# Optimization experiments

Hardware: AMD Instinct MI355X
Metric: run time of the kernel (lower is better)

Reference implementation:

```python
import jax, jax.numpy as jnp
import numpy as np

B, T, D, K, DEPTH = 8, 1024, 128, 64, 1


def _rel_ids(T, k):
    # relative_mat_id[i, j] = clamp(k + j - i, 0, 2k)
    base = jnp.arange(k, k + T)[None, :] - jnp.arange(T)[:, None]
    return jnp.clip(base, 0, 2 * k)  # [T, T] int32


def setup_inputs() -> dict:
    key = jax.random.key(0)
    ks = jax.random.split(key, 13)
    s = 1.0 / np.sqrt(D)
    return {
        "x": jax.random.normal(ks[0], (B, T, D), dtype=jnp.float32),
        "W0": jax.random.normal(ks[1], (D, D), dtype=jnp.float32) * s,
        "b0": jnp.zeros((D,), dtype=jnp.float32),
        "Wq": jax.random.normal(ks[2], (D, D), dtype=jnp.float32) * s,
        "bq": jnp.zeros((D,), dtype=jnp.float32),
        "Wk": jax.random.normal(ks[3], (D, D), dtype=jnp.float32) * s,
        "bk": jnp.zeros((D,), dtype=jnp.float32),
        "Wv": jax.random.normal(ks[4], (D, D), dtype=jnp.float32) * s,
        "bv": jnp.zeros((D,), dtype=jnp.float32),
        "W1": jax.random.normal(ks[5], (D, D), dtype=jnp.float32) * s,
        "b1": jnp.zeros((D,), dtype=jnp.float32),
        "pe_key": jax.random.normal(ks[6], (2 * K + 1, D), dtype=jnp.float32) * np.sqrt(2.0 / (2 * K + 1)),
        "pe_value": jax.random.normal(ks[7], (2 * K + 1, D), dtype=jnp.float32) * np.sqrt(2.0 / (2 * K + 1)),
    }


def reference(x, W0, b0, Wq, bq, Wk, bk, Wv, bv, W1, b1, pe_key, pe_value):
    Tlen = x.shape[1]
    ids = _rel_ids(Tlen, K)                     # [T, T]
    rpr_key = pe_key[ids]                       # [T, T, D]
    rpr_value = pe_value[ids]                   # [T, T, D]

    hs = jax.nn.relu(x @ W0 + b0)               # fc0 (dropout = eval identity)
    for _ in range(DEPTH):
        q = jnp.tanh(hs @ Wq + bq)
        k = jnp.tanh(hs @ Wk + bk)
        v = jnp.tanh(hs @ Wv + bv)
        a = jnp.einsum("bid,bjd->bij", q, k)
        a = a + jnp.einsum("ijd,bid->bij", rpr_key, q)
        a = jax.nn.softmax(a, axis=2)
        c = jnp.einsum("bij,bjd->bid", a, v)
        c = c + jnp.einsum("bij,ijd->bid", a, rpr_value)
        hs = jax.nn.relu(c @ W1 + b1)
    return hs
```

## Files before the change

kernel.cpp:

```cpp
#include <hip/hip_runtime.h>


#define TT 1024
#define DD 128
#define NB 8
#define SJH 1160

typedef _Float16 f16;
typedef __attribute__((ext_vector_type(8))) _Float16 f16x8;
typedef __attribute__((ext_vector_type(4))) _Float16 f16x4;
typedef __attribute__((ext_vector_type(4))) float f32x4;

static __device__ inline float fast_tanh(float x) {
    float xc = fminf(fmaxf(x, -12.f), 12.f);
    float e = __expf(2.f * xc);
    return (e - 1.f) / (e + 1.f);
}

#define GLDS(gp, lp) __builtin_amdgcn_global_load_lds( \
    (const __attribute__((address_space(1))) unsigned*)(gp), \
    (__attribute__((address_space(3))) unsigned*)(lp), 16, 0, 0)

__global__ __launch_bounds__(256) void prep_w(
        const float* __restrict__ W0, const float* __restrict__ Wq,
        const float* __restrict__ Wk, const float* __restrict__ Wv,
        const float* __restrict__ W1, char* __restrict__ wimg) {
    const int blk = blockIdx.x, t = threadIdx.x;
    const float* W = blk == 0 ? W0 : blk == 1 ? Wq : blk == 2 ? Wk
                   : blk == 3 ? Wv : W1;
    char* o = wimg + (size_t)blk * 32768;
    #pragma unroll
    for (int it = 0; it < 8; it++) {
        int item = t + 256 * it;
        int n = item & 127, k0 = (item >> 7) * 8;
        f16x8 h;
        #pragma unroll
        for (int e = 0; e < 8; e++) h[e] = (f16)W[(k0 + e) * 128 + n];
        *(f16x8*)(o + n * 256 + ((2 * k0) ^ ((n & 7) << 4))) = h;
    }
}

#define ZACC() do { _Pragma("unroll") for (int _i = 0; _i < 2; _i++) \
    _Pragma("unroll") for (int _j = 0; _j < 2; _j++) \
        acc[_i][_j] = (f32x4){0.f, 0.f, 0.f, 0.f}; } while (0)

#define GEMMCORE(SRC, WL) do { \
    _Pragma("unroll") for (int _c = 0; _c < 4; _c++) { \
        f16x8 _af[2], _bf[2]; \
        _Pragma("unroll") for (int _it = 0; _it < 2; _it++) { \
            int _row = _it * 16 + (l & 15); \
            int _a = (_row << 8) + (_c << 6) + ((l >> 4) << 4); \
            _af[_it] = *(const f16x8*)((SRC) + (_a ^ ((_row & 7) << 4))); } \
        _Pragma("unroll") for (int _nt = 0; _nt < 2; _nt++) { \
            int _n = wv * 32 + _nt * 16 + (l & 15); \
            int _a = (_n << 8) + (_c << 6) + ((l >> 4) << 4); \
            _bf[_nt] = *(const f16x8*)((WL) + (_a ^ ((_n & 7) << 4))); } \
        _Pragma("unroll") for (int _it = 0; _it < 2; _it++) \
        _Pragma("unroll") for (int _nt = 0; _nt < 2; _nt++) \
            acc[_it][_nt] = __builtin_amdgcn_mfma_f32_16x16x32_f16( \
                    _af[_it], _bf[_nt], acc[_it][_nt], 0, 0, 0); } } while (0)

#define ISSUEW(wi, dst) do { \
    const char* _g = wimg + (size_t)(wi) * 32768 + t * 16; \
    char* _d = (dst) + t * 16; \
    _Pragma("unroll") for (int _i = 0; _i < 8; _i++) \
        GLDS(_g + _i * 4096, _d + _i * 4096); \
} while (0)

#define WAITBAR(N) do { \
    asm volatile("s_waitcnt vmcnt(" #N ") lgkmcnt(0)" ::: "memory"); \
    __builtin_amdgcn_s_barrier(); \
    __builtin_amdgcn_sched_barrier(0); \
} while (0)

__global__ __launch_bounds__(256) void fused_qkv(
        const float* __restrict__ x, const char* __restrict__ wimg,
        const float* __restrict__ b0, const float* __restrict__ bq,
        const float* __restrict__ bk, const float* __restrict__ bv,
        const float* __restrict__ PEK, const float* __restrict__ PEV,
        f16* __restrict__ q16, char* __restrict__ kimg,
        char* __restrict__ vimg, char* __restrict__ pekimg,
        char* __restrict__ pevimg) {
    extern __shared__ __align__(16) char smq[];
    char* xs  = smq;
    char* hsl = smq + 8192;
    char* wA  = smq + 16384;
    char* wB  = smq + 49152;
    char* wC  = smq + 81920;
    const int t = threadIdx.x, wv = t >> 6, l = t & 63;
    const int blk = blockIdx.x;

    if (blk >= 256) {
        if (blk == 256) {
            for (int it = 0; it < 64; it++) {
                int idx = t + 256 * it;
                int m = idx >> 7, d = idx & 127;
                *(f16*)(pekimg + (m >> 6) * 16384 + (m & 63) * 256
                        + ((2 * d) ^ ((m & 7) << 4))) = (f16)PEK[m * 128 + d];
            }
        } else {
            for (int it = 0; it < 64; it++) {
                int idx = t + 256 * it;
                int m = idx >> 7, d = idx & 127;
                *(f16*)(pevimg + (m >> 6) * 16384 + d * 128
                        + ((2 * (m & 63)) ^ ((d & 7) << 4))) = (f16)PEV[m * 128 + d];
            }
        }
        return;
    }

    const int r0 = (blk & 7) * 1024 + (blk >> 3) * 32;
    ISSUEW(0, wA);
    ISSUEW(1, wB);
    {
        const float* X = x + (size_t)r0 * 128;
        #pragma unroll
        for (int i = 0; i < 2; i++) {
            f32x4 a0 = *(const f32x4*)(X + t * 16 + i * 8);
            f32x4 a1 = *(const f32x4*)(X + t * 16 + i * 8 + 4);
            f16x8 h;
            h[0]=(f16)a0[0]; h[1]=(f16)a0[1]; h[2]=(f16)a0[2]; h[3]=(f16)a0[3];
            h[4]=(f16)a1[0]; h[5]=(f16)a1[1]; h[6]=(f16)a1[2]; h[7]=(f16)a1[3];
            int a = t * 32 + i * 16;
            *(f16x8*)(xs + (a ^ (((a >> 8) & 7) << 4))) = h;
        }
    }
    WAITBAR(8);

    f32x4 acc[2][2];
    ZACC();
    GEMMCORE(xs, wA);
    {
        #pragma unroll
        for (int it = 0; it < 2; it++)
            #pragma unroll
            for (int nt = 0; nt < 2; nt++) {
                int n = wv * 32 + nt * 16 + (l & 15);
                float bb = b0[n];
                #pragma unroll
                for (int r = 0; r < 4; r++) {
                    int i = it * 16 + (l >> 4) * 4 + r;
                    float v = fmaxf(acc[it][nt][r] + bb, 0.f);
                    int a = i * 256 + 2 * n;
                    *(f16*)(hsl + (a ^ ((i & 7) << 4))) = (f16)v;
                }
            }
    }
    ISSUEW(2, wC);
    WAITBAR(8);

    ZACC();
    GEMMCORE(hsl, wB);
    {
        #pragma unroll
        for (int it = 0; it < 2; it++)
            #pragma unroll
            for (int nt = 0; nt < 2; nt++) {
                int n = wv * 32 + nt * 16 + (l & 15);
                float bb = bq[n];
                #pragma unroll
                for (int r = 0; r < 4; r++) {
                    int i = it * 16 + (l >> 4) * 4 + r;
                    q16[(size_t)(r0 + i) * 128 + n] =
                            (f16)fast_tanh(acc[it][nt][r] + bb);
                }
            }
    }
    ISSUEW(3, wA);
    WAITBAR(8);

    ZACC();
    GEMMCORE(hsl, wC);
    f16* ts = (f16*)xs;
    {
        #pragma unroll
        for (int it = 0; it < 2; it++)
            #pragma unroll
            for (int nt = 0; nt < 2; nt++) {
                int n = wv * 32 + nt * 16 + (l & 15);
                float bb = bk[n];
                #pragma unroll
                for (int r = 0; r < 4; r++) {
                    int i = it * 16 + (l >> 4) * 4 + r;
                    ts[i * 128 + n] = (f16)fast_tanh(acc[it][nt][r] + bb);
                }
            }
    }
    WAITBAR(0);

    {
        #pragma unroll
        for (int half = 0; half < 2; half++) {
            int row = (t >> 4) + half * 16;
            int seg = t & 15;
            int jg = r0 + row;
            int chunk = ((jg >> 10) << 4) + ((jg & 1023) >> 6);
            int jp = jg & 63;
            char* dst = kimg + (size_t)chunk * 16384 + jp * 256
                      + ((seg * 16) ^ ((jp & 7) << 4));
            *(f16x8*)dst = *(const f16x8*)&ts[row * 128 + seg * 8];
        }
    }
    ZACC();
    GEMMCORE(hsl, wA);
    {
        #pragma unroll
        for (int it = 0; it < 2; it++)
            #pragma unroll
            for (int nt = 0; nt < 2; nt++) {
                int d = wv * 32 + nt * 16 + (l & 15);
                float bb = bv[d];
                f16x4 h;
                #pragma unroll
                for (int r = 0; r < 4; r++)
                    h[r] = (f16)fast_tanh(acc[it][nt][r] + bb);
                int jb = r0 + it * 16 + ((l >> 4) << 2);
                int chunk = ((jb >> 10) << 4) + ((jb & 1023) >> 6);
                char* dst = vimg + (size_t)chunk * 16384 + d * 128
                          + ((2 * (jb & 63)) ^ ((d & 7) << 4));
                *(f16x4*)dst = h;
            }
    }
}

#define ISSUE16(src, bi) do { const char* _g = (src) + t * 16; \
    char* _d = BUF + (size_t)(bi) * 16384 + t * 16; \
    GLDS(_g, _d); \
    GLDS(_g + 8192, _d + 8192); \
} while (0)

__global__ __launch_bounds__(512) void attn_all(
        const f16* __restrict__ q16, const char* __restrict__ kimg,
        const char* __restrict__ pekimg, const char* __restrict__ vimg,
        const char* __restrict__ pevimg, const float* __restrict__ PEK,
        const float* __restrict__ PEV, const char* __restrict__ w1img,
        const float* __restrict__ b1, float* __restrict__ out) {
    extern __shared__ __align__(16) char sm7[];
    f16*   S   = (f16*)sm7;
    char*  BUF = sm7 + 74240;
    f16*   QB  = (f16*)(sm7 + 139776);
    float* LR  = (float*)(sm7 + 148224);

    const int t = threadIdx.x, wv = t >> 6, l = t & 63;
    const int lr = l & 15, lg = l >> 4;
    const int b = blockIdx.x & 7;
    const int i0 = (blockIdx.x >> 3) << 5;
    const int it16 = (wv & 1) << 4;
    const int jsub = wv >> 1;

    f16x8 qf[4];
    {
        const f16* qb = q16 + (size_t)(b * TT + i0 + it16 + lr) * 128 + lg * 8;
        #pragma unroll
        for (int c = 0; c < 4; c++) qf[c] = *(const f16x8*)(qb + c * 32);
    }
    const int row2 = t >> 4, l16 = t & 15;
    f16x8 qpv = *(const f16x8*)(q16 + (size_t)(b * TT + i0 + row2) * 128 + l16 * 8);
    f32x4 pkv0 = *(const f32x4*)(PEK + 128 * 128 + l16 * 8);
    f32x4 pkv1 = *(const f32x4*)(PEK + 128 * 128 + l16 * 8 + 4);
    f32x4 pvr4 = *(const f32x4*)(PEV + 128 * 128 + wv * 16 + lg * 4);
    const float bb1 = b1[wv * 16 + lr];

    const char* kbase = kimg + (size_t)b * 16 * 16384;
    const char* vbase = vimg + (size_t)b * 16 * 16384;

    ISSUE16(kbase, 0);
    ISSUE16(kbase + 16384, 1);
    ISSUE16(kbase + 2 * 16384, 2);

    for (int ch = 0; ch < 18; ch++) {
        asm volatile("s_waitcnt vmcnt(4)" ::: "memory");
        __builtin_amdgcn_s_barrier();
        __builtin_amdgcn_sched_barrier(0);
        {
            int ci = ch + 3;
            const char* src = ci < 16 ? kbase + (size_t)ci * 16384
                            : (ci < 18 ? pekimg + (size_t)(ci - 16) * 16384
                                       : vbase + (size_t)(ci - 18) * 16384);
            ISSUE16(src, ci & 3);
        }
        const char* kb = BUF + (size_t)(ch & 3) * 16384;
        const int jp = jsub * 16 + lr;
        f32x4 acc = {0.f, 0.f, 0.f, 0.f};
        #pragma unroll
        for (int c = 0; c < 4; c++) {
            f16x8 kf = *(const f16x8*)(kb + jp * 256
                        + ((c * 64 + lg * 16) ^ ((jp & 7) << 4)));
            acc = __builtin_amdgcn_mfma_f32_16x16x32_f16(kf, qf[c], acc, 0, 0, 0);
        }
        f16x4 h = {(f16)acc[0], (f16)acc[1], (f16)acc[2], (f16)acc[3]};
        *(f16x4*)&S[(it16 + lr) * SJH + ch * 64 + jsub * 16 + lg * 4] = h;
    }
    asm volatile("s_waitcnt lgkmcnt(0)" ::: "memory");
    __builtin_amdgcn_s_barrier();
    __builtin_amdgcn_sched_barrier(0);

    {
        const int ig = i0 + row2;
        f16* srow = S + row2 * SJH;
        f16* qrow = QB + row2 * 132;

        float qp;
        {
            float s = 0.f;
            #pragma unroll
            for (int e = 0; e < 4; e++) s += (float)qpv[e] * pkv0[e];
            #pragma unroll
            for (int e = 0; e < 4; e++) s += (float)qpv[e + 4] * pkv1[e];
            #pragma unroll
            for (int off = 8; off; off >>= 1) s += __shfl_xor(s, off, 64);
            qp = s;
        }
        for (int mm = l16; mm < 128; mm += 16) {
            qrow[mm] = srow[1024 + mm];
            srow[1024 + mm] = (f16)0.f;
        }
        if (l16 == 0) qrow[128] = (f16)qp;
        const float qlo = (float)qrow[0], qhi = qp;

        float lmax = -3.0e38f;
        #pragma unroll
        for (int kk = 0; kk < 8; kk++) {
            int j0 = kk * 128 + l16 * 8;
            f16x8 sv = *(const f16x8*)(srow + j0);
            #pragma unroll
            for (int e = 0; e < 8; e++) {
                int idd = 64 + j0 + e - ig;
                float qv = (idd <= 0) ? qlo : (idd >= 128 ? qhi : (float)qrow[idd]);
                lmax = fmaxf(lmax, (float)sv[e] + qv);
            }
        }
        #pragma unroll
        for (int off = 8; off; off >>= 1) lmax = fmaxf(lmax, __shfl_xor(lmax, off, 64));

        float lsum = 0.f, s0 = 0.f, s1 = 0.f;
        #pragma unroll
        for (int kk = 0; kk < 8; kk++) {
            int j0 = kk * 128 + l16 * 8;
            f16x8 sv = *(const f16x8*)(srow + j0);
            f16x8 pv;
            #pragma unroll
            for (int e = 0; e < 8; e++) {
                int idd = 64 + j0 + e - ig;
                float qv = (idd <= 0) ? qlo : (idd >= 128 ? qhi : (float)qrow[idd]);
                float p = __expf((float)sv[e] + qv - lmax);
                pv[e] = (f16)p;
                lsum += p;
                if (idd <= 0)        s0 += p;
                else if (idd >= 128) s1 += p;
                else                 srow[1024 + idd] = (f16)p;
            }
            *(f16x8*)(srow + j0) = pv;
        }
        #pragma unroll
        for (int off = 8; off; off >>= 1) {
            lsum += __shfl_xor(lsum, off, 64);
            s0   += __shfl_xor(s0,   off, 64);
            s1   += __shfl_xor(s1,   off, 64);
        }
        if (l16 == 0) {
            srow[1024] = (f16)s0;
            srow[1152] = (f16)s1;
            LR[row2] = lsum;
        }
    }
    asm volatile("s_waitcnt lgkmcnt(0)" ::: "memory");
    __builtin_amdgcn_s_barrier();
    __builtin_amdgcn_sched_barrier(0);

    f32x4 cacc[2] = {};
    for (int ch = 0; ch < 18; ch++) {
        if (ch <= 15)      asm volatile("s_waitcnt vmcnt(4)" ::: "memory");
        else if (ch == 16) asm volatile("s_waitcnt vmcnt(2)" ::: "memory");
        else               asm volatile("s_waitcnt vmcnt(0)" ::: "memory");
        __builtin_amdgcn_s_barrier();
        __builtin_amdgcn_sched_barrier(0);
        if (ch < 15) {
            int ci = ch + 3;
            const char* src = ci < 16 ? vbase + (size_t)ci * 16384
                                      : pevimg + (size_t)(ci - 16) * 16384;
            ISSUE16(src, (ci + 2) & 3);
        } else if (ch == 17) {
            const char* _g = w1img + t * 16;
            char* _d = BUF + t * 16;
            #pragma unroll
            for (int _i = 0; _i < 4; _i++)
                GLDS(_g + _i * 8192, _d + _i * 8192);
        }
        const char* vb = BUF + (size_t)((ch + 2) & 3) * 16384;
        const int dp = wv * 16 + lr;
        #pragma unroll
        for (int c2 = 0; c2 < 2; c2++) {
            f16x8 vf = *(const f16x8*)(vb + dp * 128
                        + ((c2 * 64 + lg * 16) ^ ((dp & 7) << 4)));
            #pragma unroll
            for (int i2 = 0; i2 < 2; i2++) {
                f16x8 pf = *(const f16x8*)&S[(i2 * 16 + lr) * SJH
                            + ch * 64 + c2 * 32 + lg * 8];
                cacc[i2] = __builtin_amdgcn_mfma_f32_16x16x32_f16(vf, pf, cacc[i2], 0, 0, 0);
            }
        }
    }

    float w128[2], rden[2];
    #pragma unroll
    for (int i2 = 0; i2 < 2; i2++) {
        int irow = i2 * 16 + lr;
        w128[i2] = (float)S[irow * SJH + 1152];
        rden[i2] = 1.f / LR[irow];
    }
    asm volatile("s_waitcnt lgkmcnt(0)" ::: "memory");
    __builtin_amdgcn_s_barrier();
    __builtin_amdgcn_sched_barrier(0);
    char* cl = (char*)S;
    {
        #pragma unroll
        for (int i2 = 0; i2 < 2; i2++) {
            int i = i2 * 16 + lr;
            #pragma unroll
            for (int r = 0; r < 4; r++) {
                int d = wv * 16 + lg * 4 + r;
                float cv = (cacc[i2][r] + w128[i2] * pvr4[r]) * rden[i2];
                int a = i * 256 + 2 * d;
                *(f16*)(cl + (a ^ ((i & 7) << 4))) = (f16)cv;
            }
        }
    }
    asm volatile("s_waitcnt vmcnt(0) lgkmcnt(0)" ::: "memory");
    __builtin_amdgcn_s_barrier();
    __builtin_amdgcn_sched_barrier(0);

    const char* wl4 = BUF;
    f32x4 oacc[2] = {};
    #pragma unroll
    for (int c = 0; c < 4; c++) {
        f16x8 af[2], bf;
        #pragma unroll
        for (int i2 = 0; i2 < 2; i2++) {
            int row = i2 * 16 + lr;
            int a = (row << 8) + (c << 6) + (lg << 4);
            af[i2] = *(const f16x8*)(cl + (a ^ ((row & 7) << 4)));
        }
        {
            int n = wv * 16 + lr;
            int a = (n << 8) + (c << 6) + (lg << 4);
            bf = *(const f16x8*)(wl4 + (a ^ ((n & 7) << 4)));
        }
        #pragma unroll
        for (int i2 = 0; i2 < 2; i2++)
            oacc[i2] = __builtin_amdgcn_mfma_f32_16x16x32_f16(af[i2], bf, oacc[i2], 0, 0, 0);
    }
    {
        int n = wv * 16 + lr;
        #pragma unroll
        for (int i2 = 0; i2 < 2; i2++) {
            #pragma unroll
            for (int r = 0; r < 4; r++) {
                int i = i2 * 16 + lg * 4 + r;
                out[(size_t)(b * TT + i0 + i) * DD + n] = fmaxf(oacc[i2][r] + bb1, 0.f);
            }
        }
    }
}


extern "C" void kernel_launch(void* const* d_in, const int* in_sizes, int n_in,
                              void* d_out, int out_size, void* d_ws, size_t ws_size,
                              hipStream_t stream) {
    const float* x   = (const float*)d_in[0];
    const float* W0  = (const float*)d_in[1];
    const float* b0  = (const float*)d_in[2];
    const float* Wq  = (const float*)d_in[3];
    const float* bq  = (const float*)d_in[4];
    const float* Wk  = (const float*)d_in[5];
    const float* bk  = (const float*)d_in[6];
    const float* Wv  = (const float*)d_in[7];
    const float* bv  = (const float*)d_in[8];
    const float* W1  = (const float*)d_in[9];
    const float* b1  = (const float*)d_in[10];
    const float* pek = (const float*)d_in[11];
    const float* pev = (const float*)d_in[12];
    float* out = (float*)d_out;

    const size_t NTD = (size_t)NB * TT * DD;
    f16* q16 = (f16*)d_ws;
    char* wimg   = (char*)(q16 + NTD);
    char* kimg   = wimg + 5 * 32768;
    char* vimg   = kimg + (size_t)128 * 16384;
    char* pekimg = vimg + (size_t)128 * 16384;
    char* pevimg = pekimg + 32768;

    const int SMEM_QKV  = 114688;
    const int SMEM_ATTN = 148352;
    hipFuncSetAttribute(reinterpret_cast<const void*>(fused_qkv),
                        hipFuncAttributeMaxDynamicSharedMemorySize, SMEM_QKV);
    hipFuncSetAttribute(reinterpret_cast<const void*>(attn_all),
                        hipFuncAttributeMaxDynamicSharedMemorySize, SMEM_ATTN);

    hipLaunchKernelGGL(prep_w, dim3(5), dim3(256), 0, stream,
                       W0, Wq, Wk, Wv, W1, wimg);
    hipLaunchKernelGGL(fused_qkv, dim3(258), dim3(256), SMEM_QKV, stream,
                       x, wimg, b0, bq, bk, bv, pek, pev,
                       q16, kimg, vimg, pekimg, pevimg);
    hipLaunchKernelGGL(attn_all, dim3(256), dim3(512), SMEM_ATTN, stream,
                       q16, kimg, pekimg, vimg, pevimg, pek, pev,
                       wimg + 4 * 32768, b1, out);
}
```

Baseline: 51.82 us.

## Fuse QKV projection and attention into one kernel with a grid barrier

Merges the QKV projection kernel and the attention kernel into a single 512-thread persistent kernel. Q stays in LDS instead of round-tripping through global memory, and a device-wide atomic-counter barrier makes sure all K/V images are written before the attention phase starts. The PE image conversion moves into the weight-prep kernel. This removes a kernel launch and the Q global traffic, but it depends on all 256 blocks being co-resident, which could deadlock otherwise, and it adds a memset launch plus spin-wait cost.

```diff
diff --git a/kernel.cpp b/kernel.cpp
--- a/kernel.cpp
+++ b/kernel.cpp
@@ -21,207 +21,68 @@
     (const __attribute__((address_space(1))) unsigned*)(gp), \
     (__attribute__((address_space(3))) unsigned*)(lp), 16, 0, 0)
 
-__global__ __launch_bounds__(256) void prep_w(
+__global__ __launch_bounds__(256) void prep_all(
         const float* __restrict__ W0, const float* __restrict__ Wq,
         const float* __restrict__ Wk, const float* __restrict__ Wv,
-        const float* __restrict__ W1, char* __restrict__ wimg) {
+        const float* __restrict__ W1, const float* __restrict__ PEK,
+        const float* __restrict__ PEV, char* __restrict__ wimg,
+        char* __restrict__ pekimg, char* __restrict__ pevimg) {
     const int blk = blockIdx.x, t = threadIdx.x;
-    const float* W = blk == 0 ? W0 : blk == 1 ? Wq : blk == 2 ? Wk
-                   : blk == 3 ? Wv : W1;
-    char* o = wimg + (size_t)blk * 32768;
-    #pragma unroll
-    for (int it = 0; it < 8; it++) {
-        int item = t + 256 * it;
-        int n = item & 127, k0 = (item >> 7) * 8;
-        f16x8 h;
-        #pragma unroll
-        for (int e = 0; e < 8; e++) h[e] = (f16)W[(k0 + e) * 128 + n];
-        *(f16x8*)(o + n * 256 + ((2 * k0) ^ ((n & 7) << 4))) = h;
+    if (blk < 5) {
+        const float* W = blk == 0 ? W0 : blk == 1 ? Wq : blk == 2 ? Wk
+                       : blk == 3 ? Wv : W1;
+        char* o = wimg + (size_t)blk * 32768;
+        #pragma unroll
+        for (int it = 0; it < 8; it++) {
+            int item = t + 256 * it;
+            int n = item & 127, k0 = (item >> 7) * 8;
+            f16x8 h;
+            #pragma unroll
+            for (int e = 0; e < 8; e++) h[e] = (f16)W[(k0 + e) * 128 + n];
+            *(f16x8*)(o + n * 256 + ((2 * k0) ^ ((n & 7) << 4))) = h;
+        }
+    } else if (blk == 5) {
+        for (int it = 0; it < 64; it++) {
+            int idx = t + 256 * it;
+            int m = idx >> 7, d = idx & 127;
+            *(f16*)(pekimg + (m >> 6) * 16384 + (m & 63) * 256
+                    + ((2 * d) ^ ((m & 7) << 4))) = (f16)PEK[m * 128 + d];
+        }
+    } else {
+        for (int it = 0; it < 64; it++) {
+            int idx = t + 256 * it;
+            int m = idx >> 7, d = idx & 127;
+            *(f16*)(pevimg + (m >> 6) * 16384 + d * 128
+                    + ((2 * (m & 63)) ^ ((d & 7) << 4))) = (f16)PEV[m * 128 + d];
+        }
     }
 }
-
-#define ZACC() do { _Pragma("unroll") for (int _i = 0; _i < 2; _i++) \
-    _Pragma("unroll") for (int _j = 0; _j < 2; _j++) \
-        acc[_i][_j] = (f32x4){0.f, 0.f, 0.f, 0.f}; } while (0)
-
-#define GEMMCORE(SRC, WL) do { \
-    _Pragma("unroll") for (int _c = 0; _c < 4; _c++) { \
-        f16x8 _af[2], _bf[2]; \
-        _Pragma("unroll") for (int _it = 0; _it < 2; _it++) { \
-            int _row = _it * 16 + (l & 15); \
-            int _a = (_row << 8) + (_c << 6) + ((l >> 4) << 4); \
-            _af[_it] = *(const f16x8*)((SRC) + (_a ^ ((_row & 7) << 4))); } \
-        _Pragma("unroll") for (int _nt = 0; _nt < 2; _nt++) { \
-            int _n = wv * 32 + _nt * 16 + (l & 15); \
-            int _a = (_n << 8) + (_c << 6) + ((l >> 4) << 4); \
-            _bf[_nt] = *(const f16x8*)((WL) + (_a ^ ((_n & 7) << 4))); } \
-        _Pragma("unroll") for (int _it = 0; _it < 2; _it++) \
-        _Pragma("unroll") for (int _nt = 0; _nt < 2; _nt++) \
-            acc[_it][_nt] = __builtin_amdgcn_mfma_f32_16x16x32_f16( \
-                    _af[_it], _bf[_nt], acc[_it][_nt], 0, 0, 0); } } while (0)
 
 #define ISSUEW(wi, dst) do { \
     const char* _g = wimg + (size_t)(wi) * 32768 + t * 16; \
     char* _d = (dst) + t * 16; \
-    _Pragma("unroll") for (int _i = 0; _i < 8; _i++) \
-        GLDS(_g + _i * 4096, _d + _i * 4096); \
+    _Pragma("unroll") for (int _i = 0; _i < 4; _i++) \
+        GLDS(_g + _i * 8192, _d + _i * 8192); \
 } while (0)
 
-#define WAITBAR(N) do { \
+#define WAITN(N) do { \
     asm volatile("s_waitcnt vmcnt(" #N ") lgkmcnt(0)" ::: "memory"); \
     __builtin_amdgcn_s_barrier(); \
     __builtin_amdgcn_sched_barrier(0); \
 } while (0)
 
-__global__ __launch_bounds__(256) void fused_qkv(
-        const float* __restrict__ x, const char* __restrict__ wimg,
-        const float* __restrict__ b0, const float* __restrict__ bq,
-        const float* __restrict__ bk, const float* __restrict__ bv,
-        const float* __restrict__ PEK, const float* __restrict__ PEV,
-        f16* __restrict__ q16, char* __restrict__ kimg,
-        char* __restrict__ vimg, char* __restrict__ pekimg,
-        char* __restrict__ pevimg) {
-    extern __shared__ __align__(16) char smq[];
-    char* xs  = smq;
-    char* hsl = smq + 8192;
-    char* wA  = smq + 16384;
-    char* wB  = smq + 49152;
-    char* wC  = smq + 81920;
-    const int t = threadIdx.x, wv = t >> 6, l = t & 63;
-    const int blk = blockIdx.x;
-
-    if (blk >= 256) {
-        if (blk == 256) {
-            for (int it = 0; it < 64; it++) {
-                int idx = t + 256 * it;
-                int m = idx >> 7, d = idx & 127;
-                *(f16*)(pekimg + (m >> 6) * 16384 + (m & 63) * 256
-                        + ((2 * d) ^ ((m & 7) << 4))) = (f16)PEK[m * 128 + d];
-            }
-        } else {
-            for (int it = 0; it < 64; it++) {
-                int idx = t + 256 * it;
-                int m = idx >> 7, d = idx & 127;
-                *(f16*)(pevimg + (m >> 6) * 16384 + d * 128
-                        + ((2 * (m & 63)) ^ ((d & 7) << 4))) = (f16)PEV[m * 128 + d];
-            }
-        }
-        return;
-    }
-
-    const int r0 = (blk & 7) * 1024 + (blk >> 3) * 32;
-    ISSUEW(0, wA);
-    ISSUEW(1, wB);
-    {
-        const float* X = x + (size_t)r0 * 128;
-        #pragma unroll
-        for (int i = 0; i < 2; i++) {
-            f32x4 a0 = *(const f32x4*)(X + t * 16 + i * 8);
-            f32x4 a1 = *(const f32x4*)(X + t * 16 + i * 8 + 4);
-            f16x8 h;
-            h[0]=(f16)a0[0]; h[1]=(f16)a0[1]; h[2]=(f16)a0[2]; h[3]=(f16)a0[3];
-            h[4]=(f16)a1[0]; h[5]=(f16)a1[1]; h[6]=(f16)a1[2]; h[7]=(f16)a1[3];
-            int a = t * 32 + i * 16;
-            *(f16x8*)(xs + (a ^ (((a >> 8) & 7) << 4))) = h;
-        }
-    }
-    WAITBAR(8);
-
-    f32x4 acc[2][2];
-    ZACC();
-    GEMMCORE(xs, wA);
-    {
-        #pragma unroll
-        for (int it = 0; it < 2; it++)
-            #pragma unroll
-            for (int nt = 0; nt < 2; nt++) {
-                int n = wv * 32 + nt * 16 + (l & 15);
-                float bb = b0[n];
-                #pragma unroll
-                for (int r = 0; r < 4; r++) {
-                    int i = it * 16 + (l >> 4) * 4 + r;
-                    float v = fmaxf(acc[it][nt][r] + bb, 0.f);
-                    int a = i * 256 + 2 * n;
-                    *(f16*)(hsl + (a ^ ((i & 7) << 4))) = (f16)v;
-                }
-            }
-    }
-    ISSUEW(2, wC);
-    WAITBAR(8);
-
-    ZACC();
-    GEMMCORE(hsl, wB);
-    {
-        #pragma unroll
-        for (int it = 0; it < 2; it++)
-            #pragma unroll
-            for (int nt = 0; nt < 2; nt++) {
-                int n = wv * 32 + nt * 16 + (l & 15);
-                float bb = bq[n];
-                #pragma unroll
-                for (int r = 0; r < 4; r++) {
-                    int i = it * 16 + (l >> 4) * 4 + r;
-                    q16[(size_t)(r0 + i) * 128 + n] =
-                            (f16)fast_tanh(acc[it][nt][r] + bb);
-                }
-            }
-    }
-    ISSUEW(3, wA);
-    WAITBAR(8);
-
-    ZACC();
-    GEMMCORE(hsl, wC);
-    f16* ts = (f16*)xs;
-    {
-        #pragma unroll
-        for (int it = 0; it < 2; it++)
-            #pragma unroll
-            for (int nt = 0; nt < 2; nt++) {
-                int n = wv * 32 + nt * 16 + (l & 15);
-                float bb = bk[n];
-                #pragma unroll
-                for (int r = 0; r < 4; r++) {
-                    int i = it * 16 + (l >> 4) * 4 + r;
-                    ts[i * 128 + n] = (f16)fast_tanh(acc[it][nt][r] + bb);
-                }
-            }
-    }
-    WAITBAR(0);
-
-    {
-        #pragma unroll
-        for (int half = 0; half < 2; half++) {
-            int row = (t >> 4) + half * 16;
-            int seg = t & 15;
-            int jg = r0 + row;
-            int chunk = ((jg >> 10) << 4) + ((jg & 1023) >> 6);
-            int jp = jg & 63;
-            char* dst = kimg + (size_t)chunk * 16384 + jp * 256
-                      + ((seg * 16) ^ ((jp & 7) << 4));
-            *(f16x8*)dst = *(const f16x8*)&ts[row * 128 + seg * 8];
-        }
-    }
-    ZACC();
-    GEMMCORE(hsl, wA);
-    {
-        #pragma unroll
-        for (int it = 0; it < 2; it++)
-            #pragma unroll
-            for (int nt = 0; nt < 2; nt++) {
-                int d = wv * 32 + nt * 16 + (l & 15);
-                float bb = bv[d];
-                f16x4 h;
-                #pragma unroll
-                for (int r = 0; r < 4; r++)
-                    h[r] = (f16)fast_tanh(acc[it][nt][r] + bb);
-                int jb = r0 + it * 16 + ((l >> 4) << 2);
-                int chunk = ((jb >> 10) << 4) + ((jb & 1023) >> 6);
-                char* dst = vimg + (size_t)chunk * 16384 + d * 128
-                          + ((2 * (jb & 63)) ^ ((d & 7) << 4));
-                *(f16x4*)dst = h;
-            }
-    }
-}
+#define GEMM8(SRC, WL) do { \
+    _Pragma("unroll") for (int _c = 0; _c < 4; _c++) { \
+        int _ar = it * 16 + lr; \
+        int _aa = (_ar << 8) + (_c << 6) + (lg << 4); \
+        f16x8 _af = *(const f16x8*)((SRC) + (_aa ^ ((_ar & 7) << 4))); \
+        _Pragma("unroll") for (int _nt = 0; _nt < 2; _nt++) { \
+            int _n = nq * 32 + _nt * 16 + lr; \
+            int _ba = (_n << 8) + (_c << 6) + (lg << 4); \
+            f16x8 _bf = *(const f16x8*)((WL) + (_ba ^ ((_n & 7) << 4))); \
+            acc[_nt] = __builtin_amdgcn_mfma_f32_16x16x32_f16( \
+                    _af, _bf, acc[_nt], 0, 0, 0); \
+        } } } while (0)
 
 #define ISSUE16(src, bi) do { const char* _g = (src) + t * 16; \
     char* _d = BUF + (size_t)(bi) * 16384 + t * 16; \
@@ -229,33 +90,157 @@
     GLDS(_g + 8192, _d + 8192); \
 } while (0)
 
-__global__ __launch_bounds__(512) void attn_all(
-        const f16* __restrict__ q16, const char* __restrict__ kimg,
-        const char* __restrict__ pekimg, const char* __restrict__ vimg,
-        const char* __restrict__ pevimg, const float* __restrict__ PEK,
-        const float* __restrict__ PEV, const char* __restrict__ w1img,
-        const float* __restrict__ b1, float* __restrict__ out) {
-    extern __shared__ __align__(16) char sm7[];
-    f16*   S   = (f16*)sm7;
-    char*  BUF = sm7 + 74240;
-    f16*   QB  = (f16*)(sm7 + 139776);
-    float* LR  = (float*)(sm7 + 148224);
-
+__global__ __launch_bounds__(512) void fused_all(
+        const float* __restrict__ x, const char* __restrict__ wimg,
+        const float* __restrict__ b0v, const float* __restrict__ bqv,
+        const float* __restrict__ bkv, const float* __restrict__ bvv,
+        const float* __restrict__ PEK, const float* __restrict__ PEV,
+        char* __restrict__ kimg, char* __restrict__ vimg,
+        const char* __restrict__ pekimg, const char* __restrict__ pevimg,
+        const float* __restrict__ b1, unsigned* __restrict__ syncc,
+        float* __restrict__ out) {
+    extern __shared__ __align__(16) char sm[];
     const int t = threadIdx.x, wv = t >> 6, l = t & 63;
     const int lr = l & 15, lg = l >> 4;
-    const int b = blockIdx.x & 7;
-    const int i0 = (blockIdx.x >> 3) << 5;
+    const int blk = blockIdx.x;
+    const int b = blk & 7, slice = blk >> 3;
+    const int r0 = b * 1024 + slice * 32;
+    const int it = wv & 1, nq = wv >> 1;
+
+    char* xs   = sm;
+    char* hsl  = sm + 8192;
+    char* wA   = sm + 16384;
+    char* wB   = sm + 49152;
+    char* wC   = sm + 81920;
+    char* qlds = sm + 139776;
+
+    ISSUEW(0, wA);
+    ISSUEW(1, wB);
+    {
+        const float* X = x + (size_t)r0 * 128 + t * 8;
+        f32x4 a0 = *(const f32x4*)X;
+        f32x4 a1 = *(const f32x4*)(X + 4);
+        f16x8 h;
+        h[0]=(f16)a0[0]; h[1]=(f16)a0[1]; h[2]=(f16)a0[2]; h[3]=(f16)a0[3];
+        h[4]=(f16)a1[0]; h[5]=(f16)a1[1]; h[6]=(f16)a1[2]; h[7]=(f16)a1[3];
+        int a = t * 16;
+        *(f16x8*)(xs + (a ^ (((a >> 8) & 7) << 4))) = h;
+    }
+    WAITN(4);
+
+    f32x4 acc[2];
+    acc[0] = (f32x4){0,0,0,0}; acc[1] = (f32x4){0,0,0,0};
+    GEMM8(xs, wA);
+    #pragma unroll
+    for (int nt = 0; nt < 2; nt++) {
+        int n = nq * 32 + nt * 16 + lr;
+        float bb = b0v[n];
+        #pragma unroll
+        for (int r = 0; r < 4; r++) {
+            int i = it * 16 + lg * 4 + r;
+            float v = fmaxf(acc[nt][r] + bb, 0.f);
+            int a = i * 256 + 2 * n;
+            *(f16*)(hsl + (a ^ ((i & 7) << 4))) = (f16)v;
+        }
+    }
+    ISSUEW(2, wC);
+    WAITN(4);
+
+    acc[0] = (f32x4){0,0,0,0}; acc[1] = (f32x4){0,0,0,0};
+    GEMM8(hsl, wB);
+    #pragma unroll
+    for (int nt = 0; nt < 2; nt++) {
+        int n = nq * 32 + nt * 16 + lr;
+        float bb = bqv[n];
+        #pragma unroll
+        for (int r = 0; r < 4; r++) {
+            int i = it * 16 + lg * 4 + r;
+            int a = i * 256 + 2 * n;
+            *(f16*)(qlds + (a ^ ((i & 7) << 4))) =
+                    (f16)fast_tanh(acc[nt][r] + bb);
+        }
+    }
+    ISSUEW(3, wA);
+    WAITN(4);
+
+    acc[0] = (f32x4){0,0,0,0}; acc[1] = (f32x4){0,0,0,0};
+    GEMM8(hsl, wC);
+    f16* ts = (f16*)xs;
+    #pragma unroll
+    for (int nt = 0; nt < 2; nt++) {
+        int n = nq * 32 + nt * 16 + lr;
+        float bb = bkv[n];
+        #pragma unroll
+        for (int r = 0; r < 4; r++) {
+            int i = it * 16 + lg * 4 + r;
+            ts[i * 128 + n] = (f16)fast_tanh(acc[nt][r] + bb);
+        }
+    }
+    asm volatile("s_waitcnt lgkmcnt(0)" ::: "memory");
+    __builtin_amdgcn_s_barrier();
+    __builtin_amdgcn_sched_barrier(0);
+    {
+        int row = t >> 4, seg = t & 15;
+        int jg = r0 + row;
+        int chunk = ((jg >> 10) << 4) + ((jg & 1023) >> 6);
+        int jp = jg & 63;
+        *(f16x8*)(kimg + (size_t)chunk * 16384 + jp * 256
+                  + ((seg * 16) ^ ((jp & 7) << 4))) =
+                *(const f16x8*)&ts[row * 128 + seg * 8];
+    }
+    WAITN(1);
+
+    acc[0] = (f32x4){0,0,0,0}; acc[1] = (f32x4){0,0,0,0};
+    GEMM8(hsl, wA);
+    #pragma unroll
+    for (int nt = 0; nt < 2; nt++) {
+        int d = nq * 32 + nt * 16 + lr;
+        float bb = bvv[d];
+        f16x4 h;
+        #pragma unroll
+        for (int r = 0; r < 4; r++) h[r] = (f16)fast_tanh(acc[nt][r] + bb);
+        int jb = r0 + it * 16 + lg * 4;
+        int chunk = ((jb >> 10) << 4) + ((jb & 1023) >> 6);
+        *(f16x4*)(vimg + (size_t)chunk * 16384 + d * 128
+                  + ((2 * (jb & 63)) ^ ((d & 7) << 4))) = h;
+    }
+
+    asm volatile("s_waitcnt vmcnt(0) lgkmcnt(0)" ::: "memory");
+    __syncthreads();
+    if (t == 0) {
+        __threadfence();
+        __hip_atomic_fetch_add(syncc, 1u, __ATOMIC_ACQ_REL,
+                               __HIP_MEMORY_SCOPE_AGENT);
+        while (__hip_atomic_load(syncc, __ATOMIC_RELAXED,
+                                 __HIP_MEMORY_SCOPE_AGENT) < 256u)
+            __builtin_amdgcn_s_sleep(2);
+        (void)__hip_atomic_load(syncc, __ATOMIC_ACQUIRE,
+                                __HIP_MEMORY_SCOPE_AGENT);
+    }
+    __syncthreads();
+
+    f16*   S   = (f16*)sm;
+    char*  BUF = sm + 74240;
+    f16*   QB  = (f16*)(sm + 139776);
+    float* LR  = (float*)(sm + 148224);
+
+    const int i0 = slice << 5;
     const int it16 = (wv & 1) << 4;
     const int jsub = wv >> 1;
 
     f16x8 qf[4];
+    #pragma unroll
+    for (int c = 0; c < 4; c++) {
+        int row = it16 + lr;
+        int a = row * 256 + c * 64 + lg * 16;
+        qf[c] = *(const f16x8*)(qlds + (a ^ ((row & 7) << 4)));
+    }
+    const int row2 = t >> 4, l16 = t & 15;
+    f16x8 qpv;
     {
-        const f16* qb = q16 + (size_t)(b * TT + i0 + it16 + lr) * 128 + lg * 8;
-        #pragma unroll
-        for (int c = 0; c < 4; c++) qf[c] = *(const f16x8*)(qb + c * 32);
-    }
-    const int row2 = t >> 4, l16 = t & 15;
-    f16x8 qpv = *(const f16x8*)(q16 + (size_t)(b * TT + i0 + row2) * 128 + l16 * 8);
+        int a = row2 * 256 + l16 * 16;
+        qpv = *(const f16x8*)(qlds + (a ^ ((row2 & 7) << 4)));
+    }
     f32x4 pkv0 = *(const f32x4*)(PEK + 128 * 128 + l16 * 8);
     f32x4 pkv1 = *(const f32x4*)(PEK + 128 * 128 + l16 * 8 + 4);
     f32x4 pvr4 = *(const f32x4*)(PEV + 128 * 128 + wv * 16 + lg * 4);
@@ -263,6 +248,9 @@
 
     const char* kbase = kimg + (size_t)b * 16 * 16384;
     const char* vbase = vimg + (size_t)b * 16 * 16384;
+
+    asm volatile("s_waitcnt lgkmcnt(0)" ::: "memory");
+    __builtin_amdgcn_s_barrier();
 
     ISSUE16(kbase, 0);
     ISSUE16(kbase + 16384, 1);
@@ -281,14 +269,14 @@
         }
         const char* kb = BUF + (size_t)(ch & 3) * 16384;
         const int jp = jsub * 16 + lr;
-        f32x4 acc = {0.f, 0.f, 0.f, 0.f};
+        f32x4 a2 = {0.f, 0.f, 0.f, 0.f};
         #pragma unroll
         for (int c = 0; c < 4; c++) {
             f16x8 kf = *(const f16x8*)(kb + jp * 256
                         + ((c * 64 + lg * 16) ^ ((jp & 7) << 4)));
-            acc = __builtin_amdgcn_mfma_f32_16x16x32_f16(kf, qf[c], acc, 0, 0, 0);
-        }
-        f16x4 h = {(f16)acc[0], (f16)acc[1], (f16)acc[2], (f16)acc[3]};
+            a2 = __builtin_amdgcn_mfma_f32_16x16x32_f16(kf, qf[c], a2, 0, 0, 0);
+        }
+        f16x4 h = {(f16)a2[0], (f16)a2[1], (f16)a2[2], (f16)a2[3]};
         *(f16x4*)&S[(it16 + lr) * SJH + ch * 64 + jsub * 16 + lg * 4] = h;
     }
     asm volatile("s_waitcnt lgkmcnt(0)" ::: "memory");
@@ -381,7 +369,7 @@
                                       : pevimg + (size_t)(ci - 16) * 16384;
             ISSUE16(src, (ci + 2) & 3);
         } else if (ch == 17) {
-            const char* _g = w1img + t * 16;
+            const char* _g = wimg + 4 * 32768 + t * 16;
             char* _d = BUF + t * 16;
             #pragma unroll
             for (int _i = 0; _i < 4; _i++)
@@ -413,17 +401,15 @@
     __builtin_amdgcn_s_barrier();
     __builtin_amdgcn_sched_barrier(0);
     char* cl = (char*)S;
-    {
-        #pragma unroll
-        for (int i2 = 0; i2 < 2; i2++) {
-            int i = i2 * 16 + lr;
-            #pragma unroll
-            for (int r = 0; r < 4; r++) {
-                int d = wv * 16 + lg * 4 + r;
-                float cv = (cacc[i2][r] + w128[i2] * pvr4[r]) * rden[i2];
-                int a = i * 256 + 2 * d;
-                *(f16*)(cl + (a ^ ((i & 7) << 4))) = (f16)cv;
-            }
+    #pragma unroll
+    for (int i2 = 0; i2 < 2; i2++) {
+        int i = i2 * 16 + lr;
+        #pragma unroll
+        for (int r = 0; r < 4; r++) {
+            int d = wv * 16 + lg * 4 + r;
+            float cv = (cacc[i2][r] + w128[i2] * pvr4[r]) * rden[i2];
+            int a = i * 256 + 2 * d;
+            *(f16*)(cl + (a ^ ((i & 7) << 4))) = (f16)cv;
         }
     }
     asm volatile("s_waitcnt vmcnt(0) lgkmcnt(0)" ::: "memory");
@@ -482,27 +468,21 @@
     const float* pev = (const float*)d_in[12];
     float* out = (float*)d_out;
 
-    const size_t NTD = (size_t)NB * TT * DD;
-    f16* q16 = (f16*)d_ws;
-    char* wimg   = (char*)(q16 + NTD);
+    char* wimg   = (char*)d_ws;
     char* kimg   = wimg + 5 * 32768;
     char* vimg   = kimg + (size_t)128 * 16384;
     char* pekimg = vimg + (size_t)128 * 16384;
     char* pevimg = pekimg + 32768;
-
-    const int SMEM_QKV  = 114688;
-    const int SMEM_ATTN = 148352;
-    hipFuncSetAttribute(reinterpret_cast<const void*>(fused_qkv),
-                        hipFuncAttributeMaxDynamicSharedMemorySize, SMEM_QKV);
-    hipFuncSetAttribute(reinterpret_cast<const void*>(attn_all),
-                        hipFuncAttributeMaxDynamicSharedMemorySize, SMEM_ATTN);
-
-    hipLaunchKernelGGL(prep_w, dim3(5), dim3(256), 0, stream,
-                       W0, Wq, Wk, Wv, W1, wimg);
-    hipLaunchKernelGGL(fused_qkv, dim3(258), dim3(256), SMEM_QKV, stream,
-                       x, wimg, b0, bq, bk, bv, pek, pev,
-                       q16, kimg, vimg, pekimg, pevimg);
-    hipLaunchKernelGGL(attn_all, dim3(256), dim3(512), SMEM_ATTN, stream,
-                       q16, kimg, pekimg, vimg, pevimg, pek, pev,
-                       wimg + 4 * 32768, b1, out);
+    unsigned* syncc = (unsigned*)(pevimg + 32768);
+
+    const int SMEM = 148352;
+    hipFuncSetAttribute(reinterpret_cast<const void*>(fused_all),
+                        hipFuncAttributeMaxDynamicSharedMemorySize, SMEM);
+
+    hipMemsetAsync(syncc, 0, sizeof(unsigned), stream);
+    hipLaunchKernelGGL(prep_all, dim3(7), dim3(256), 0, stream,
+                       W0, Wq, Wk, Wv, W1, pek, pev, wimg, pekimg, pevimg);
+    hipLaunchKernelGGL(fused_all, dim3(256), dim3(512), SMEM, stream,
+                       x, wimg, b0, bq, bk, bv, pek, pev, kimg, vimg,
+                       pekimg, pevimg, b1, syncc, out);
 }
```

Result: slower. 64.05 us (+23.6%).

## Halve attention block tile to 16 query rows, doubling grid and cutting LDS

Applied to the files above, without the earlier changes.

The attention kernel now processes 16 query rows per block with 4 waves instead of 32 rows with 8 waves, so the grid doubles to 512 blocks and LDS use is roughly halved. The K/V streaming pipeline moves from 4 buffers (3 in flight) to 2 buffers, with a full vmcnt(0) wait each chunk. PE table conversion moves out of fused_qkv into the weight-prep kernel. The aim is more resident blocks per CU and better occupancy. The cost is that each block re-streams all of K/V for half the rows, doubling global and L2 traffic, and the shallower prefetch exposes more load latency.

```diff
diff --git a/kernel.cpp b/kernel.cpp
--- a/kernel.cpp
+++ b/kernel.cpp
@@ -21,22 +21,40 @@
     (const __attribute__((address_space(1))) unsigned*)(gp), \
     (__attribute__((address_space(3))) unsigned*)(lp), 16, 0, 0)
 
-__global__ __launch_bounds__(256) void prep_w(
+__global__ __launch_bounds__(256) void prep_all(
         const float* __restrict__ W0, const float* __restrict__ Wq,
         const float* __restrict__ Wk, const float* __restrict__ Wv,
-        const float* __restrict__ W1, char* __restrict__ wimg) {
+        const float* __restrict__ W1, const float* __restrict__ PEK,
+        const float* __restrict__ PEV, char* __restrict__ wimg,
+        char* __restrict__ pekimg, char* __restrict__ pevimg) {
     const int blk = blockIdx.x, t = threadIdx.x;
-    const float* W = blk == 0 ? W0 : blk == 1 ? Wq : blk == 2 ? Wk
-                   : blk == 3 ? Wv : W1;
-    char* o = wimg + (size_t)blk * 32768;
-    #pragma unroll
-    for (int it = 0; it < 8; it++) {
-        int item = t + 256 * it;
-        int n = item & 127, k0 = (item >> 7) * 8;
-        f16x8 h;
-        #pragma unroll
-        for (int e = 0; e < 8; e++) h[e] = (f16)W[(k0 + e) * 128 + n];
-        *(f16x8*)(o + n * 256 + ((2 * k0) ^ ((n & 7) << 4))) = h;
+    if (blk < 5) {
+        const float* W = blk == 0 ? W0 : blk == 1 ? Wq : blk == 2 ? Wk
+                       : blk == 3 ? Wv : W1;
+        char* o = wimg + (size_t)blk * 32768;
+        #pragma unroll
+        for (int it = 0; it < 8; it++) {
+            int item = t + 256 * it;
+            int n = item & 127, k0 = (item >> 7) * 8;
+            f16x8 h;
+            #pragma unroll
+            for (int e = 0; e < 8; e++) h[e] = (f16)W[(k0 + e) * 128 + n];
+            *(f16x8*)(o + n * 256 + ((2 * k0) ^ ((n & 7) << 4))) = h;
+        }
+    } else if (blk == 5) {
+        for (int it = 0; it < 64; it++) {
+            int idx = t + 256 * it;
+            int m = idx >> 7, d = idx & 127;
+            *(f16*)(pekimg + (m >> 6) * 16384 + (m & 63) * 256
+                    + ((2 * d) ^ ((m & 7) << 4))) = (f16)PEK[m * 128 + d];
+        }
+    } else {
+        for (int it = 0; it < 64; it++) {
+            int idx = t + 256 * it;
+            int m = idx >> 7, d = idx & 127;
+            *(f16*)(pevimg + (m >> 6) * 16384 + d * 128
+                    + ((2 * (m & 63)) ^ ((d & 7) << 4))) = (f16)PEV[m * 128 + d];
+        }
     }
 }
 
@@ -77,10 +95,8 @@
         const float* __restrict__ x, const char* __restrict__ wimg,
         const float* __restrict__ b0, const float* __restrict__ bq,
         const float* __restrict__ bk, const float* __restrict__ bv,
-        const float* __restrict__ PEK, const float* __restrict__ PEV,
         f16* __restrict__ q16, char* __restrict__ kimg,
-        char* __restrict__ vimg, char* __restrict__ pekimg,
-        char* __restrict__ pevimg) {
+        char* __restrict__ vimg) {
     extern __shared__ __align__(16) char smq[];
     char* xs  = smq;
     char* hsl = smq + 8192;
@@ -89,25 +105,6 @@
     char* wC  = smq + 81920;
     const int t = threadIdx.x, wv = t >> 6, l = t & 63;
     const int blk = blockIdx.x;
-
-    if (blk >= 256) {
-        if (blk == 256) {
-            for (int it = 0; it < 64; it++) {
-                int idx = t + 256 * it;
-                int m = idx >> 7, d = idx & 127;
-                *(f16*)(pekimg + (m >> 6) * 16384 + (m & 63) * 256
-                        + ((2 * d) ^ ((m & 7) << 4))) = (f16)PEK[m * 128 + d];
-            }
-        } else {
-            for (int it = 0; it < 64; it++) {
-                int idx = t + 256 * it;
-                int m = idx >> 7, d = idx & 127;
-                *(f16*)(pevimg + (m >> 6) * 16384 + d * 128
-                        + ((2 * (m & 63)) ^ ((d & 7) << 4))) = (f16)PEV[m * 128 + d];
-            }
-        }
-        return;
-    }
 
     const int r0 = (blk & 7) * 1024 + (blk >> 3) * 32;
     ISSUEW(0, wA);
@@ -225,11 +222,11 @@
 
 #define ISSUE16(src, bi) do { const char* _g = (src) + t * 16; \
     char* _d = BUF + (size_t)(bi) * 16384 + t * 16; \
-    GLDS(_g, _d); \
-    GLDS(_g + 8192, _d + 8192); \
+    GLDS(_g, _d); GLDS(_g + 4096, _d + 4096); \
+    GLDS(_g + 8192, _d + 8192); GLDS(_g + 12288, _d + 12288); \
 } while (0)
 
-__global__ __launch_bounds__(512) void attn_all(
+__global__ __launch_bounds__(256) void attn_all(
         const f16* __restrict__ q16, const char* __restrict__ kimg,
         const char* __restrict__ pekimg, const char* __restrict__ vimg,
         const char* __restrict__ pevimg, const float* __restrict__ PEK,
@@ -237,20 +234,18 @@
         const float* __restrict__ b1, float* __restrict__ out) {
     extern __shared__ __align__(16) char sm7[];
     f16*   S   = (f16*)sm7;
-    char*  BUF = sm7 + 74240;
-    f16*   QB  = (f16*)(sm7 + 139776);
-    float* LR  = (float*)(sm7 + 148224);
+    char*  BUF = sm7 + 37120;
+    f16*   QB  = (f16*)(sm7 + 69888);
+    float* LR  = (float*)(sm7 + 74112);
 
     const int t = threadIdx.x, wv = t >> 6, l = t & 63;
     const int lr = l & 15, lg = l >> 4;
     const int b = blockIdx.x & 7;
-    const int i0 = (blockIdx.x >> 3) << 5;
-    const int it16 = (wv & 1) << 4;
-    const int jsub = wv >> 1;
+    const int i0 = (blockIdx.x >> 3) << 4;
 
     f16x8 qf[4];
     {
-        const f16* qb = q16 + (size_t)(b * TT + i0 + it16 + lr) * 128 + lg * 8;
+        const f16* qb = q16 + (size_t)(b * TT + i0 + lr) * 128 + lg * 8;
         #pragma unroll
         for (int c = 0; c < 4; c++) qf[c] = *(const f16x8*)(qb + c * 32);
     }
@@ -258,38 +253,41 @@
     f16x8 qpv = *(const f16x8*)(q16 + (size_t)(b * TT + i0 + row2) * 128 + l16 * 8);
     f32x4 pkv0 = *(const f32x4*)(PEK + 128 * 128 + l16 * 8);
     f32x4 pkv1 = *(const f32x4*)(PEK + 128 * 128 + l16 * 8 + 4);
-    f32x4 pvr4 = *(const f32x4*)(PEV + 128 * 128 + wv * 16 + lg * 4);
-    const float bb1 = b1[wv * 16 + lr];
+    f32x4 pvr4[2];
+    #pragma unroll
+    for (int dt = 0; dt < 2; dt++)
+        pvr4[dt] = *(const f32x4*)(PEV + 128 * 128 + wv * 32 + dt * 16 + lg * 4);
+    float bb1[2];
+    #pragma unroll
+    for (int nt = 0; nt < 2; nt++) bb1[nt] = b1[wv * 32 + nt * 16 + lr];
 
     const char* kbase = kimg + (size_t)b * 16 * 16384;
     const char* vbase = vimg + (size_t)b * 16 * 16384;
 
     ISSUE16(kbase, 0);
-    ISSUE16(kbase + 16384, 1);
-    ISSUE16(kbase + 2 * 16384, 2);
 
     for (int ch = 0; ch < 18; ch++) {
-        asm volatile("s_waitcnt vmcnt(4)" ::: "memory");
+        asm volatile("s_waitcnt vmcnt(0)" ::: "memory");
         __builtin_amdgcn_s_barrier();
         __builtin_amdgcn_sched_barrier(0);
         {
-            int ci = ch + 3;
+            int ci = ch + 1;
             const char* src = ci < 16 ? kbase + (size_t)ci * 16384
                             : (ci < 18 ? pekimg + (size_t)(ci - 16) * 16384
-                                       : vbase + (size_t)(ci - 18) * 16384);
-            ISSUE16(src, ci & 3);
-        }
-        const char* kb = BUF + (size_t)(ch & 3) * 16384;
-        const int jp = jsub * 16 + lr;
-        f32x4 acc = {0.f, 0.f, 0.f, 0.f};
+                                       : vbase);
+            ISSUE16(src, ci & 1);
+        }
+        const char* kb = BUF + (size_t)(ch & 1) * 16384;
+        const int jp = wv * 16 + lr;
+        f32x4 a2 = {0.f, 0.f, 0.f, 0.f};
         #pragma unroll
         for (int c = 0; c < 4; c++) {
             f16x8 kf = *(const f16x8*)(kb + jp * 256
                         + ((c * 64 + lg * 16) ^ ((jp & 7) << 4)));
-            acc = __builtin_amdgcn_mfma_f32_16x16x32_f16(kf, qf[c], acc, 0, 0, 0);
-        }
-        f16x4 h = {(f16)acc[0], (f16)acc[1], (f16)acc[2], (f16)acc[3]};
-        *(f16x4*)&S[(it16 + lr) * SJH + ch * 64 + jsub * 16 + lg * 4] = h;
+            a2 = __builtin_amdgcn_mfma_f32_16x16x32_f16(kf, qf[c], a2, 0, 0, 0);
+        }
+        f16x4 h = {(f16)a2[0], (f16)a2[1], (f16)a2[2], (f16)a2[3]};
+        *(f16x4*)&S[lr * SJH + ch * 64 + wv * 16 + lg * 4] = h;
     }
     asm volatile("s_waitcnt lgkmcnt(0)" ::: "memory");
     __builtin_amdgcn_s_barrier();
@@ -370,60 +368,54 @@
 
     f32x4 cacc[2] = {};
     for (int ch = 0; ch < 18; ch++) {
-        if (ch <= 15)      asm volatile("s_waitcnt vmcnt(4)" ::: "memory");
-        else if (ch == 16) asm volatile("s_waitcnt vmcnt(2)" ::: "memory");
-        else               asm volatile("s_waitcnt vmcnt(0)" ::: "memory");
+        asm volatile("s_waitcnt vmcnt(0)" ::: "memory");
         __builtin_amdgcn_s_barrier();
         __builtin_amdgcn_sched_barrier(0);
-        if (ch < 15) {
-            int ci = ch + 3;
-            const char* src = ci < 16 ? vbase + (size_t)ci * 16384
-                                      : pevimg + (size_t)(ci - 16) * 16384;
-            ISSUE16(src, (ci + 2) & 3);
-        } else if (ch == 17) {
-            const char* _g = w1img + t * 16;
-            char* _d = BUF + t * 16;
-            #pragma unroll
-            for (int _i = 0; _i < 4; _i++)
-                GLDS(_g + _i * 8192, _d + _i * 8192);
-        }
-        const char* vb = BUF + (size_t)((ch + 2) & 3) * 16384;
-        const int dp = wv * 16 + lr;
+        {
+            int ci = ch + 1;
+            if (ci < 16)      ISSUE16(vbase + (size_t)ci * 16384, ci & 1);
+            else if (ci < 18) ISSUE16(pevimg + (size_t)(ci - 16) * 16384, ci & 1);
+            else {
+                const char* _g = w1img + t * 16;
+                char* _d = BUF + t * 16;
+                GLDS(_g, _d); GLDS(_g + 4096, _d + 4096);
+                GLDS(_g + 8192, _d + 8192); GLDS(_g + 12288, _d + 12288);
+            }
+        }
+        const char* vb = BUF + (size_t)(ch & 1) * 16384;
         #pragma unroll
         for (int c2 = 0; c2 < 2; c2++) {
-            f16x8 vf = *(const f16x8*)(vb + dp * 128
-                        + ((c2 * 64 + lg * 16) ^ ((dp & 7) << 4)));
-            #pragma unroll
-            for (int i2 = 0; i2 < 2; i2++) {
-                f16x8 pf = *(const f16x8*)&S[(i2 * 16 + lr) * SJH
-                            + ch * 64 + c2 * 32 + lg * 8];
-                cacc[i2] = __builtin_amdgcn_mfma_f32_16x16x32_f16(vf, pf, cacc[i2], 0, 0, 0);
-            }
-        }
-    }
-
-    float w128[2], rden[2];
-    #pragma unroll
-    for (int i2 = 0; i2 < 2; i2++) {
-        int irow = i2 * 16 + lr;
-        w128[i2] = (float)S[irow * SJH + 1152];
-        rden[i2] = 1.f / LR[irow];
-    }
+            f16x8 pf = *(const f16x8*)&S[lr * SJH + ch * 64 + c2 * 32 + lg * 8];
+            #pragma unroll
+            for (int dt = 0; dt < 2; dt++) {
+                int dp = wv * 32 + dt * 16 + lr;
+                f16x8 vf = *(const f16x8*)(vb + dp * 128
+                            + ((c2 * 64 + lg * 16) ^ ((dp & 7) << 4)));
+                cacc[dt] = __builtin_amdgcn_mfma_f32_16x16x32_f16(vf, pf, cacc[dt], 0, 0, 0);
+            }
+        }
+    }
+
+    const float w128 = (float)S[lr * SJH + 1152];
+    const float rden = 1.f / LR[lr];
     asm volatile("s_waitcnt lgkmcnt(0)" ::: "memory");
     __builtin_amdgcn_s_barrier();
     __builtin_amdgcn_sched_barrier(0);
+    {
+        const char* _g = w1img + 16384 + t * 16;
+        char* _d = BUF + 16384 + t * 16;
+        GLDS(_g, _d); GLDS(_g + 4096, _d + 4096);
+        GLDS(_g + 8192, _d + 8192); GLDS(_g + 12288, _d + 12288);
+    }
     char* cl = (char*)S;
-    {
-        #pragma unroll
-        for (int i2 = 0; i2 < 2; i2++) {
-            int i = i2 * 16 + lr;
-            #pragma unroll
-            for (int r = 0; r < 4; r++) {
-                int d = wv * 16 + lg * 4 + r;
-                float cv = (cacc[i2][r] + w128[i2] * pvr4[r]) * rden[i2];
-                int a = i * 256 + 2 * d;
-                *(f16*)(cl + (a ^ ((i & 7) << 4))) = (f16)cv;
-            }
+    #pragma unroll
+    for (int dt = 0; dt < 2; dt++) {
+        #pragma unroll
+        for (int r = 0; r < 4; r++) {
+            int d = wv * 32 + dt * 16 + lg * 4 + r;
+            float cv = (cacc[dt][r] + w128 * pvr4[dt][r]) * rden;
+            int a = lr * 256 + 2 * d;
+            *(f16*)(cl + (a ^ ((lr & 7) << 4))) = (f16)cv;
         }
     }
     asm volatile("s_waitcnt vmcnt(0) lgkmcnt(0)" ::: "memory");
@@ -434,31 +426,23 @@
     f32x4 oacc[2] = {};
     #pragma unroll
     for (int c = 0; c < 4; c++) {
-        f16x8 af[2], bf;
-        #pragma unroll
-        for (int i2 = 0; i2 < 2; i2++) {
-            int row = i2 * 16 + lr;
-            int a = (row << 8) + (c << 6) + (lg << 4);
-            af[i2] = *(const f16x8*)(cl + (a ^ ((row & 7) << 4)));
-        }
-        {
-            int n = wv * 16 + lr;
-            int a = (n << 8) + (c << 6) + (lg << 4);
-            bf = *(const f16x8*)(wl4 + (a ^ ((n & 7) << 4)));
-        }
-        #pragma unroll
-        for (int i2 = 0; i2 < 2; i2++)
-            oacc[i2] = __builtin_amdgcn_mfma_f32_16x16x32_f16(af[i2], bf, oacc[i2], 0, 0, 0);
-    }
-    {
-        int n = wv * 16 + lr;
-        #pragma unroll
-        for (int i2 = 0; i2 < 2; i2++) {
-            #pragma unroll
-            for (int r = 0; r < 4; r++) {
-                int i = i2 * 16 + lg * 4 + r;
-                out[(size_t)(b * TT + i0 + i) * DD + n] = fmaxf(oacc[i2][r] + bb1, 0.f);
-            }
+        int aa = lr * 256 + c * 64 + lg * 16;
+        f16x8 af = *(const f16x8*)(cl + (aa ^ ((lr & 7) << 4)));
+        #pragma unroll
+        for (int nt = 0; nt < 2; nt++) {
+            int n = wv * 32 + nt * 16 + lr;
+            int ba = n * 256 + c * 64 + lg * 16;
+            f16x8 bf = *(const f16x8*)(wl4 + (ba ^ ((n & 7) << 4)));
+            oacc[nt] = __builtin_amdgcn_mfma_f32_16x16x32_f16(af, bf, oacc[nt], 0, 0, 0);
+        }
+    }
+    #pragma unroll
+    for (int nt = 0; nt < 2; nt++) {
+        int n = wv * 32 + nt * 16 + lr;
+        #pragma unroll
+        for (int r = 0; r < 4; r++) {
+            int i = lg * 4 + r;
+            out[(size_t)(b * TT + i0 + i) * DD + n] = fmaxf(oacc[nt][r] + bb1[nt], 0.f);
         }
     }
 }
@@ -483,7 +467,7 @@
     float* out = (float*)d_out;
 
     const size_t NTD = (size_t)NB * TT * DD;
-    f16* q16 = (f16*)d_ws;
+    f16* q16     = (f16*)d_ws;
     char* wimg   = (char*)(q16 + NTD);
     char* kimg   = wimg + 5 * 32768;
     char* vimg   = kimg + (size_t)128 * 16384;
@@ -491,18 +475,17 @@
     char* pevimg = pekimg + 32768;
 
     const int SMEM_QKV  = 114688;
-    const int SMEM_ATTN = 148352;
+    const int SMEM_ATTN = 74176;
     hipFuncSetAttribute(reinterpret_cast<const void*>(fused_qkv),
                         hipFuncAttributeMaxDynamicSharedMemorySize, SMEM_QKV);
     hipFuncSetAttribute(reinterpret_cast<const void*>(attn_all),
                         hipFuncAttributeMaxDynamicSharedMemorySize, SMEM_ATTN);
 
-    hipLaunchKernelGGL(prep_w, dim3(5), dim3(256), 0, stream,
-                       W0, Wq, Wk, Wv, W1, wimg);
-    hipLaunchKernelGGL(fused_qkv, dim3(258), dim3(256), SMEM_QKV, stream,
-                       x, wimg, b0, bq, bk, bv, pek, pev,
-                       q16, kimg, vimg, pekimg, pevimg);
-    hipLaunchKernelGGL(attn_all, dim3(256), dim3(512), SMEM_ATTN, stream,
+    hipLaunchKernelGGL(prep_all, dim3(7), dim3(256), 0, stream,
+                       W0, Wq, Wk, Wv, W1, pek, pev, wimg, pekimg, pevimg);
+    hipLaunchKernelGGL(fused_qkv, dim3(256), dim3(256), SMEM_QKV, stream,
+                       x, wimg, b0, bq, bk, bv, q16, kimg, vimg);
+    hipLaunchKernelGGL(attn_all, dim3(512), dim3(256), SMEM_ATTN, stream,
                        q16, kimg, pekimg, vimg, pevimg, pek, pev,
                        wimg + 4 * 32768, b1, out);
 }
```

Result: faster. 50.76 us (-2.0%).
